# Performance work log

Measured on AMD Instinct MI355X. Metric: run time of the kernel, lower is better.

## Reference

```python
import jax, jax.numpy as jnp
import numpy as np

O, I, B = 4096, 4096, 4096  # out_features, in_features, flattened tokens
GROUP = 128
INIT_PEAK = 2.0


def setup_inputs() -> dict:
    key = jax.random.key(0)
    k1, k2, k3, k4 = jax.random.split(key, 4)
    x = jax.random.normal(k1, (B, I), jnp.float32)
    # initial_ternary in {-1,0,1} -> theta init per the torch constructor
    tern = jax.random.randint(k2, (O, I), -1, 2)
    theta_neg = jnp.where(tern == -1, INIT_PEAK, -INIT_PEAK).astype(jnp.float32)
    theta_pos = jnp.where(tern == 1, INIT_PEAK, -INIT_PEAK).astype(jnp.float32)
    # per-group scales expanded to full weight shape (scales.unsqueeze(1).expand.reshape)
    n_groups = O * I // GROUP
    scales = jax.random.uniform(k3, (n_groups,), jnp.float32, 0.01, 0.05)
    scales_exp = jnp.repeat(scales, GROUP).reshape(O, I)
    # reparameterization noise (training path), made explicit for determinism
    eps = jax.random.normal(k4, (B, O), jnp.float32)
    return {"x": x, "theta_neg": theta_neg, "theta_pos": theta_pos,
            "scales_exp": scales_exp, "eps": eps}


def reference(x, theta_neg, theta_pos, scales_exp, eps):
    # stable 3-way softmax over logits [theta_neg, 0, theta_pos], done without
    # materializing the stacked [O, I, 3] tensor
    m = jnp.maximum(jnp.maximum(theta_neg, theta_pos), 0.0)
    e_neg = jnp.exp(theta_neg - m)
    e_zero = jnp.exp(-m)
    e_pos = jnp.exp(theta_pos - m)
    Z = e_neg + e_zero + e_pos
    p_neg = e_neg / Z
    p_pos = e_pos / Z
    diff = p_pos - p_neg
    w_mean = diff * scales_exp                                   # [O, I]
    w_var = (p_pos + p_neg - diff * diff) * (scales_exp * scales_exp)  # [O, I]
    mu = x @ w_mean.T                                            # [B, O]
    sigma_sq = (x * x) @ w_var.T                                 # [B, O]
    sigma = jnp.sqrt(jnp.maximum(sigma_sq, 1e-8))
    return mu + sigma * eps
```

## Files before the change

kernel.cpp:

```cpp
#include <hip/hip_runtime.h>

#define I_DIM 4096
#define O_DIM 4096
#define B_DIM 4096

typedef _Float16 f16;
typedef __attribute__((ext_vector_type(8))) _Float16 f16x8;
typedef __attribute__((ext_vector_type(4))) float f32x4;

struct f16pair { f16 m, v; };

__device__ inline f16pair lr_wmv(float tn, float tp, float s) {
    float m = fmaxf(fmaxf(tn, tp), 0.0f);
    float en = __expf(tn - m);
    float ez = __expf(-m);
    float ep = __expf(tp - m);
    float inv = __builtin_amdgcn_rcpf(en + ez + ep);
    float pn = en * inv, pp = ep * inv;
    float d = pp - pn;
    f16pair r;
    r.m = (f16)(d * s);
    r.v = (f16)((pp + pn - d * d) * (s * s));
    return r;
}

__global__ void prep_all(const float4* __restrict__ x, f16x8* __restrict__ xb8,
                         const float4* __restrict__ tn4, const float4* __restrict__ tp4,
                         const float4* __restrict__ sc4,
                         f16x8* __restrict__ wm8, f16x8* __restrict__ wv8,
                         int nbx) {
    const int bid = blockIdx.x;
    if (bid < nbx) {
        size_t i = (size_t)bid * blockDim.x + threadIdx.x;
        float4 a = x[2 * i];
        float4 b = x[2 * i + 1];
        f16x8 o;
        o[0] = (f16)a.x; o[1] = (f16)a.y; o[2] = (f16)a.z; o[3] = (f16)a.w;
        o[4] = (f16)b.x; o[5] = (f16)b.y; o[6] = (f16)b.z; o[7] = (f16)b.w;
        xb8[i] = o;
    } else {
        size_t i = (size_t)(bid - nbx) * blockDim.x + threadIdx.x;
        float4 a0 = tn4[2 * i], a1 = tn4[2 * i + 1];
        float4 b0 = tp4[2 * i], b1 = tp4[2 * i + 1];
        float4 s0 = sc4[2 * i], s1 = sc4[2 * i + 1];
        f16x8 om, ov;
        f16pair p;
        p = lr_wmv(a0.x, b0.x, s0.x); om[0] = p.m; ov[0] = p.v;
        p = lr_wmv(a0.y, b0.y, s0.y); om[1] = p.m; ov[1] = p.v;
        p = lr_wmv(a0.z, b0.z, s0.z); om[2] = p.m; ov[2] = p.v;
        p = lr_wmv(a0.w, b0.w, s0.w); om[3] = p.m; ov[3] = p.v;
        p = lr_wmv(a1.x, b1.x, s1.x); om[4] = p.m; ov[4] = p.v;
        p = lr_wmv(a1.y, b1.y, s1.y); om[5] = p.m; ov[5] = p.v;
        p = lr_wmv(a1.z, b1.z, s1.z); om[6] = p.m; ov[6] = p.v;
        p = lr_wmv(a1.w, b1.w, s1.w); om[7] = p.m; ov[7] = p.v;
        wm8[i] = om;
        wv8[i] = ov;
    }
}

#define BM 128
#define BN 128
#define BK 64

__device__ inline void gl_lds16(const f16* g, f16* l) {
    __builtin_amdgcn_global_load_lds(
        (const __attribute__((address_space(1))) unsigned int*)g,
        (__attribute__((address_space(3))) unsigned int*)l,
        16, 0, 0);
}

__global__ __launch_bounds__(256, 2)
void fused_dual_gemm(const f16* __restrict__ Xb,
                     const f16* __restrict__ Wm, const f16* __restrict__ Wv,
                     const float* __restrict__ eps, float* __restrict__ out) {
    __shared__ f16 smem[24576];
    f16* sX  = smem;

    const int tid  = threadIdx.x;
    const int lane = tid & 63;
    const int wave = tid >> 6;

    const int bm = blockIdx.y * BM;
    const int bn = blockIdx.x * BN;

    const int rowoff = lane >> 3;
    const int cgoff  = ((lane & 7) ^ rowoff) << 3;

    const f16* g[12];
    int loff[12];
#pragma unroll
    for (int j = 0; j < 12; ++j) {
        const int cj  = wave + 4 * j;
        const int arr = cj >> 4;
        const int lc  = cj & 15;
        const int tb  = (arr == 0) ? bm : bn;
        const f16* base = (arr == 0) ? Xb : ((arr == 1) ? Wm : Wv);
        g[j] = base + (size_t)(tb + lc * 8 + rowoff) * I_DIM + cgoff;
        loff[j] = cj << 9;
    }

    const int fr  = lane & 15;
    const int sw0 = (((lane >> 4) ^ (fr & 7)) << 3);
    const int m0 = (wave >> 1) << 6;
    const int n0 = (wave & 1) << 6;

    f32x4 accM[4][4];
    f32x4 accV[4][4];
    const f32x4 z = {0.0f, 0.0f, 0.0f, 0.0f};
#pragma unroll
    for (int mi = 0; mi < 4; ++mi)
#pragma unroll
        for (int ni = 0; ni < 4; ++ni) { accM[mi][ni] = z; accV[mi][ni] = z; }

    const f16* sWm = smem + 8192;
    const f16* sWv = smem + 16384;

    for (int k0 = 0; k0 < I_DIM; k0 += BK) {
        __syncthreads();
#pragma unroll
        for (int j = 0; j < 12; ++j)
            gl_lds16(g[j] + k0, smem + loff[j]);
        __syncthreads();

#pragma unroll
        for (int kh = 0; kh < 2; ++kh) {
            const int sw = sw0 ^ (kh << 5);
            f16x8 a[4], a2[4];
#pragma unroll
            for (int mi = 0; mi < 4; ++mi) {
                a[mi]  = *(const f16x8*)&sX[(m0 + mi * 16 + fr) * BK + sw];
                a2[mi] = a[mi] * a[mi];
            }
#pragma unroll
            for (int ni = 0; ni < 4; ++ni) {
                const int rowb = (n0 + ni * 16 + fr) * BK + sw;
                f16x8 bm_ = *(const f16x8*)&sWm[rowb];
                f16x8 bv_ = *(const f16x8*)&sWv[rowb];
#pragma unroll
                for (int mi = 0; mi < 4; ++mi) {
                    accM[mi][ni] = __builtin_amdgcn_mfma_f32_16x16x32_f16(
                        a[mi], bm_, accM[mi][ni], 0, 0, 0);
                    accV[mi][ni] = __builtin_amdgcn_mfma_f32_16x16x32_f16(
                        a2[mi], bv_, accV[mi][ni], 0, 0, 0);
                }
            }
        }
    }

    const int oc  = lane & 15;
    const int orb = (lane >> 4) << 2;
#pragma unroll
    for (int mi = 0; mi < 4; ++mi) {
#pragma unroll
        for (int ni = 0; ni < 4; ++ni) {
            const int gn = bn + n0 + ni * 16 + oc;
            const int gm = bm + m0 + mi * 16 + orb;
#pragma unroll
            for (int r = 0; r < 4; ++r) {
                const size_t off = (size_t)(gm + r) * O_DIM + gn;
                const float mu = accM[mi][ni][r];
                const float vv = accV[mi][ni][r];
                out[off] = fmaf(sqrtf(fmaxf(vv, 1e-8f)), eps[off], mu);
            }
        }
    }
}

extern "C" void kernel_launch(void* const* d_in, const int* in_sizes, int n_in,
                              void* d_out, int out_size, void* d_ws, size_t ws_size,
                              hipStream_t stream) {
    const float* x   = (const float*)d_in[0];
    const float* tn  = (const float*)d_in[1];
    const float* tp  = (const float*)d_in[2];
    const float* sc  = (const float*)d_in[3];
    const float* eps = (const float*)d_in[4];
    float* out = (float*)d_out;

    const size_t NE = (size_t)O_DIM * I_DIM;
    f16* xb = (f16*)d_ws;
    f16* wm = xb + NE;
    f16* wv = wm + NE;

    const int nbx = (int)(NE / 8 / 256);
    const int nbw = (int)(NE / 8 / 256);
    prep_all<<<nbx + nbw, 256, 0, stream>>>(
        (const float4*)x, (f16x8*)xb,
        (const float4*)tn, (const float4*)tp, (const float4*)sc,
        (f16x8*)wm, (f16x8*)wv, nbx);

    dim3 grid(O_DIM / BN, B_DIM / BM);
    fused_dual_gemm<<<grid, 256, 0, stream>>>(
        (const f16*)xb, (const f16*)wm, (const f16*)wv, eps, out);
}
```

Before: 540.1 us.

## Pipeline dual GEMM with 4-stage LDS ring buffer and 256-row tiles over 8 waves

Turns the single-buffer load-sync-compute loop into a software-pipelined schedule: a ring of four 32-wide K slices in LDS, async global-to-LDS loads issued ahead and tracked with explicit vmcnt waits, and MFMA phases interleaved with staging of later slices. The block tile grows to 256 rows with 512 threads so each W tile is reused across more X rows. The aim is to hide global memory latency and cut barrier stalls, at the cost of 128 KB of LDS per block, which may limit occupancy, and hand-tuned waitcnt logic that is fragile.

```diff
diff --git a/kernel.cpp b/kernel.cpp
--- a/kernel.cpp
+++ b/kernel.cpp
@@ -58,7 +58,7 @@
     }
 }
 
-#define BM 128
+#define BM 256
 #define BN 128
 #define BK 64
 
@@ -69,12 +69,17 @@
         16, 0, 0);
 }
 
-__global__ __launch_bounds__(256, 2)
+#define VM8 asm volatile("s_waitcnt vmcnt(8)")
+#define VM6 asm volatile("s_waitcnt vmcnt(6)")
+#define VM4 asm volatile("s_waitcnt vmcnt(4)")
+#define VM0 asm volatile("s_waitcnt vmcnt(0)")
+#define VMNONE (void)0
+
+__global__ __launch_bounds__(512, 2)
 void fused_dual_gemm(const f16* __restrict__ Xb,
                      const f16* __restrict__ Wm, const f16* __restrict__ Wv,
                      const float* __restrict__ eps, float* __restrict__ out) {
-    __shared__ f16 smem[24576];
-    f16* sX  = smem;
+    __shared__ f16 smem[65536];
 
     const int tid  = threadIdx.x;
     const int lane = tid & 63;
@@ -83,24 +88,16 @@
     const int bm = blockIdx.y * BM;
     const int bn = blockIdx.x * BN;
 
-    const int rowoff = lane >> 3;
-    const int cgoff  = ((lane & 7) ^ rowoff) << 3;
-
-    const f16* g[12];
-    int loff[12];
-#pragma unroll
-    for (int j = 0; j < 12; ++j) {
-        const int cj  = wave + 4 * j;
-        const int arr = cj >> 4;
-        const int lc  = cj & 15;
-        const int tb  = (arr == 0) ? bm : bn;
-        const f16* base = (arr == 0) ? Xb : ((arr == 1) ? Wm : Wv);
-        g[j] = base + (size_t)(tb + lc * 8 + rowoff) * I_DIM + cgoff;
-        loff[j] = cj << 9;
-    }
+    const int srow = lane >> 2;
+    const int scol = (((lane & 3) ^ ((lane >> 3) & 3)) << 3);
+    const f16* gX = Xb + (size_t)(bm + 32 * wave + srow) * I_DIM + scol;
+    const f16* gM = Wm + (size_t)(bn + 16 * wave + srow) * I_DIM + scol;
+    const f16* gV = Wv + (size_t)(bn + 16 * wave + srow) * I_DIM + scol;
+    f16* ldsX = smem + wave * 1024;
+    f16* ldsW = smem + 16384 + wave * 512;
 
     const int fr  = lane & 15;
-    const int sw0 = (((lane >> 4) ^ (fr & 7)) << 3);
+    const int sg8 = (((lane >> 4) ^ ((fr >> 1) & 3)) << 3);
     const int m0 = (wave >> 1) << 6;
     const int n0 = (wave & 1) << 6;
 
@@ -112,40 +109,73 @@
 #pragma unroll
         for (int ni = 0; ni < 4; ++ni) { accM[mi][ni] = z; accV[mi][ni] = z; }
 
-    const f16* sWm = smem + 8192;
-    const f16* sWv = smem + 16384;
-
-    for (int k0 = 0; k0 < I_DIM; k0 += BK) {
-        __syncthreads();
-#pragma unroll
-        for (int j = 0; j < 12; ++j)
-            gl_lds16(g[j] + k0, smem + loff[j]);
-        __syncthreads();
-
-#pragma unroll
-        for (int kh = 0; kh < 2; ++kh) {
-            const int sw = sw0 ^ (kh << 5);
-            f16x8 a[4], a2[4];
-#pragma unroll
-            for (int mi = 0; mi < 4; ++mi) {
-                a[mi]  = *(const f16x8*)&sX[(m0 + mi * 16 + fr) * BK + sw];
-                a2[mi] = a[mi] * a[mi];
-            }
-#pragma unroll
-            for (int ni = 0; ni < 4; ++ni) {
-                const int rowb = (n0 + ni * 16 + fr) * BK + sw;
-                f16x8 bm_ = *(const f16x8*)&sWm[rowb];
-                f16x8 bv_ = *(const f16x8*)&sWv[rowb];
-#pragma unroll
-                for (int mi = 0; mi < 4; ++mi) {
-                    accM[mi][ni] = __builtin_amdgcn_mfma_f32_16x16x32_f16(
-                        a[mi], bm_, accM[mi][ni], 0, 0, 0);
-                    accV[mi][ni] = __builtin_amdgcn_mfma_f32_16x16x32_f16(
-                        a2[mi], bv_, accV[mi][ni], 0, 0, 0);
-                }
-            }
-        }
+    f16x8 a[4], a2[4];
+
+#define STAGE_X(kelem, reg) do {                                               \
+        gl_lds16(gX + (kelem),              ldsX + (reg));                     \
+        gl_lds16(gX + (kelem) + 16 * I_DIM, ldsX + (reg) + 512);               \
+    } while (0)
+#define STAGE_W(kelem, reg) do {                                               \
+        gl_lds16(gM + (kelem), ldsW + (reg));                                  \
+        gl_lds16(gV + (kelem), ldsW + (reg) + 4096);                           \
+    } while (0)
+
+#define PHASE(RX, RW, NH, STG, VM) do {                                        \
+        if ((NH) == 0) {                                                       \
+            _Pragma("unroll")                                                  \
+            for (int mi = 0; mi < 4; ++mi) {                                   \
+                a[mi]  = *(const f16x8*)(smem + (RX) + (m0 + mi * 16 + fr) * 32 + sg8); \
+                a2[mi] = a[mi] * a[mi];                                        \
+            }                                                                  \
+        }                                                                      \
+        const f16x8 b0m = *(const f16x8*)(smem + (RW)        + (n0 + ((NH) * 2 + 0) * 16 + fr) * 32 + sg8); \
+        const f16x8 b0v = *(const f16x8*)(smem + (RW) + 4096 + (n0 + ((NH) * 2 + 0) * 16 + fr) * 32 + sg8); \
+        const f16x8 b1m = *(const f16x8*)(smem + (RW)        + (n0 + ((NH) * 2 + 1) * 16 + fr) * 32 + sg8); \
+        const f16x8 b1v = *(const f16x8*)(smem + (RW) + 4096 + (n0 + ((NH) * 2 + 1) * 16 + fr) * 32 + sg8); \
+        STG;                                                                   \
+        __builtin_amdgcn_s_barrier();                                          \
+        asm volatile("s_waitcnt lgkmcnt(0)");                                  \
+        __builtin_amdgcn_sched_barrier(0);                                     \
+        __builtin_amdgcn_s_setprio(1);                                         \
+        _Pragma("unroll")                                                      \
+        for (int mi = 0; mi < 4; ++mi) {                                       \
+            accM[mi][(NH) * 2 + 0] = __builtin_amdgcn_mfma_f32_16x16x32_f16(a[mi],  b0m, accM[mi][(NH) * 2 + 0], 0, 0, 0); \
+            accV[mi][(NH) * 2 + 0] = __builtin_amdgcn_mfma_f32_16x16x32_f16(a2[mi], b0v, accV[mi][(NH) * 2 + 0], 0, 0, 0); \
+            accM[mi][(NH) * 2 + 1] = __builtin_amdgcn_mfma_f32_16x16x32_f16(a[mi],  b1m, accM[mi][(NH) * 2 + 1], 0, 0, 0); \
+            accV[mi][(NH) * 2 + 1] = __builtin_amdgcn_mfma_f32_16x16x32_f16(a2[mi], b1v, accV[mi][(NH) * 2 + 1], 0, 0, 0); \
+        }                                                                      \
+        __builtin_amdgcn_s_setprio(0);                                         \
+        VM;                                                                    \
+        __builtin_amdgcn_s_barrier();                                          \
+    } while (0)
+
+    STAGE_X(0, 0);      STAGE_W(0, 0);
+    STAGE_X(32, 8192);  STAGE_W(32, 8192);
+    STAGE_X(64, 32768); STAGE_W(64, 32768);
+    VM8;
+    __builtin_amdgcn_s_barrier();
+
+#pragma unroll 1
+    for (int i = 0; i < 31; ++i) {
+        const int kb = i * 128;
+        PHASE(0,     16384, 0, STAGE_X(kb +  96, 40960), VMNONE);
+        PHASE(0,     16384, 1, STAGE_W(kb +  96, 40960), VM6);
+        PHASE(8192,  24576, 0, STAGE_X(kb + 128,     0), VMNONE);
+        PHASE(8192,  24576, 1, STAGE_W(kb + 128,     0), VM6);
+        PHASE(32768, 49152, 0, STAGE_X(kb + 160,  8192), VMNONE);
+        PHASE(32768, 49152, 1, STAGE_W(kb + 160,  8192), VM6);
+        PHASE(40960, 57344, 0, STAGE_X(kb + 192, 32768), VMNONE);
+        PHASE(40960, 57344, 1, STAGE_W(kb + 192, 32768), VM6);
     }
+
+    PHASE(0,     16384, 0, STAGE_X(4064, 40960), VMNONE);
+    PHASE(0,     16384, 1, STAGE_W(4064, 40960), VM6);
+    PHASE(8192,  24576, 0, VMNONE, VMNONE);
+    PHASE(8192,  24576, 1, VMNONE, VM4);
+    PHASE(32768, 49152, 0, VMNONE, VMNONE);
+    PHASE(32768, 49152, 1, VMNONE, VM0);
+    PHASE(40960, 57344, 0, VMNONE, VMNONE);
+    PHASE(40960, 57344, 1, VMNONE, VMNONE);
 
     const int oc  = lane & 15;
     const int orb = (lane >> 4) << 2;
@@ -164,6 +194,9 @@
             }
         }
     }
+#undef PHASE
+#undef STAGE_X
+#undef STAGE_W
 }
 
 extern "C" void kernel_launch(void* const* d_in, const int* in_sizes, int n_in,
@@ -189,6 +222,6 @@
         (f16x8*)wm, (f16x8*)wv, nbx);
 
     dim3 grid(O_DIM / BN, B_DIM / BM);
-    fused_dual_gemm<<<grid, 256, 0, stream>>>(
+    fused_dual_gemm<<<grid, 512, 0, stream>>>(
         (const f16*)xb, (const f16*)wm, (const f16*)wv, eps, out);
 }
```

New measurement: 545.4 us. No clear change (+1.0%).
